# Kernel tuning notes

Hardware: AMD Instinct MI355X
Metric: run time of the kernel (lower is better)

Reference implementation:

```python
import jax, jax.numpy as jnp
import numpy as np

B, T = 64, 16384          # batch, frame_length
M, K = 8, 3               # memory_length, degree


def setup_inputs() -> dict:
    key = jax.random.key(0)
    k1, k2 = jax.random.split(key)
    x = jax.random.normal(k1, (B, T, 2), dtype=jnp.float32)
    h_0 = jnp.zeros((1,), dtype=jnp.float32)  # unused by the module, kept for signature fidelity
    Weight = jax.random.normal(k2, (M, 1 + K * M), dtype=jnp.float32) * 0.1
    return {"x": x, "h_0": h_0, "Weight": Weight}


def _gmp_forward(x, Weight):
    Bm, Tn, _ = x.shape
    Mm, Wd = Weight.shape
    Kk = (Wd - 1) // Mm
    cdt = jnp.complex64
    xc = jax.lax.complex(x[..., 0], x[..., 1])               # (B, T) complex
    zp = jnp.zeros((Bm, Mm - 1), dtype=cdt)
    xp = jnp.concatenate([zp, xc], axis=1)                   # (B, T+M-1): x padded by M-1 zeros
    # original code pads AGAIN before abs -> amp has a 2*(M-1)-zero prefix
    ap = jnp.abs(jnp.concatenate([zp, xp], axis=1))          # (B, T+2M-2) real
    # amp^(d+1) for d = 0..K-1  -> (B, K, T+2M-2)
    powers = ap[:, None, :] ** jnp.arange(1, Kk + 1, dtype=ap.dtype)[None, :, None]
    # sliding windows of xp: WX[b, j, i] = xp[b, j+i], i = 0..M-1  -> (B, T, M)
    WX = jnp.stack([xp[:, i:i + Tn] for i in range(Mm)], axis=-1)
    # Weight[:, 0] multiplies the raw window; Weight[:, 1:] reshaped to [tap i, lag m, degree d]
    W3 = Weight[:, 1:].reshape(Mm, Mm, Kk)
    out = jnp.einsum('i,bji->bj', Weight[:, 0].astype(cdt), WX)
    for m in range(Mm):  # structural loop over memory lags (M is small & fixed)
        # PWm[b, d, j, i] = amp_pad[b, j+m+i]^(d+1)  -> (B, K, T, M)
        PWm = jnp.stack([powers[:, :, m + i:m + i + Tn] for i in range(Mm)], axis=-1)
        out = out + jnp.einsum('bji,bdji,id->bj', WX, PWm.astype(cdt), W3[:, m, :].astype(cdt))
    return jnp.stack([jnp.real(out), jnp.imag(out)], axis=-1)  # (B, T, 2)


def reference(x, h_0, Weight):
    return _gmp_forward(x, Weight)
```

## Files before the change

kernel.cpp:

```cpp
#include <hip/hip_runtime.h>


#define B_SZ 64
#define T_SZ 16384
#define M_SZ 8
#define K_SZ 3
#define CHUNK 256
#define HALO 14
#define WIN (CHUNK + HALO)

__global__ __launch_bounds__(256) void gmp_kernel(const float* __restrict__ x,
                                                  const float* __restrict__ W,
                                                  float* __restrict__ out) {
    __shared__ float xre[WIN], xim[WIN], a1[WIN], a2[WIN], a3[WIN];
    const int tid   = threadIdx.x;
    const int chunk = blockIdx.x & 63;
    const int b     = blockIdx.x >> 6;
    const int j0    = chunk * CHUNK;

    for (int q = tid; q < WIN; q += 256) {
        const int g = j0 - HALO + q;
        float re = 0.f, im = 0.f;
        if (g >= 0) {
            const float2 v = ((const float2*)x)[(size_t)b * T_SZ + g];
            re = v.x; im = v.y;
        }
        const float s2 = fmaf(re, re, im * im);
        const float s1 = sqrtf(s2);
        xre[q] = re; xim[q] = im;
        a1[q] = s1; a2[q] = s2; a3[q] = s2 * s1;
    }
    __syncthreads();

    float accr = 0.f, acci = 0.f;
#pragma unroll
    for (int i = 0; i < M_SZ; ++i) {
        float c = W[i * 25];
#pragma unroll
        for (int m = 0; m < M_SZ; ++m) {
            const int q = tid + i + m;
            const int wb = i * 25 + 1 + m * 3;
            c = fmaf(W[wb + 0], a1[q], c);
            c = fmaf(W[wb + 1], a2[q], c);
            c = fmaf(W[wb + 2], a3[q], c);
        }
        const int qx = tid + i + 7;
        accr = fmaf(xre[qx], c, accr);
        acci = fmaf(xim[qx], c, acci);
    }

    const int j = j0 + tid;
    ((float2*)out)[(size_t)b * T_SZ + j] = make_float2(accr, acci);
}

extern "C" void kernel_launch(void* const* d_in, const int* in_sizes, int n_in,
                              void* d_out, int out_size, void* d_ws, size_t ws_size,
                              hipStream_t stream) {
    const float* x = (const float*)d_in[0];
    const float* W = (const float*)d_in[2];
    float* out = (float*)d_out;
    const int grid = B_SZ * (T_SZ / CHUNK);
    gmp_kernel<<<dim3(grid), dim3(256), 0, stream>>>(x, W, out);
}
```

Baseline: 70.51 us.

## Compute two outputs per thread with register-cached windows and Horner powers

```diff
diff --git a/kernel.cpp b/kernel.cpp
--- a/kernel.cpp
+++ b/kernel.cpp
@@ -3,54 +3,59 @@
 
 #define B_SZ 64
 #define T_SZ 16384
-#define M_SZ 8
-#define K_SZ 3
-#define CHUNK 256
+#define CHUNK 512
 #define HALO 14
 #define WIN (CHUNK + HALO)
 
 __global__ __launch_bounds__(256) void gmp_kernel(const float* __restrict__ x,
                                                   const float* __restrict__ W,
                                                   float* __restrict__ out) {
-    __shared__ float xre[WIN], xim[WIN], a1[WIN], a2[WIN], a3[WIN];
+    __shared__ float2 xs[WIN];
+    __shared__ float  as[WIN];
     const int tid   = threadIdx.x;
-    const int chunk = blockIdx.x & 63;
-    const int b     = blockIdx.x >> 6;
+    const int chunk = blockIdx.x & 31;
+    const int b     = blockIdx.x >> 5;
     const int j0    = chunk * CHUNK;
 
     for (int q = tid; q < WIN; q += 256) {
         const int g = j0 - HALO + q;
-        float re = 0.f, im = 0.f;
-        if (g >= 0) {
-            const float2 v = ((const float2*)x)[(size_t)b * T_SZ + g];
-            re = v.x; im = v.y;
-        }
-        const float s2 = fmaf(re, re, im * im);
-        const float s1 = sqrtf(s2);
-        xre[q] = re; xim[q] = im;
-        a1[q] = s1; a2[q] = s2; a3[q] = s2 * s1;
+        float2 v = make_float2(0.f, 0.f);
+        if (g >= 0) v = ((const float2*)x)[(size_t)b * T_SZ + g];
+        xs[q] = v;
+        as[q] = sqrtf(fmaf(v.x, v.x, v.y * v.y));
     }
     __syncthreads();
 
-    float accr = 0.f, acci = 0.f;
+    float av[16];
 #pragma unroll
-    for (int i = 0; i < M_SZ; ++i) {
-        float c = W[i * 25];
+    for (int k = 0; k < 16; ++k) av[k] = as[2 * tid + k];
+    float2 xv[9];
 #pragma unroll
-        for (int m = 0; m < M_SZ; ++m) {
-            const int q = tid + i + m;
-            const int wb = i * 25 + 1 + m * 3;
-            c = fmaf(W[wb + 0], a1[q], c);
-            c = fmaf(W[wb + 1], a2[q], c);
-            c = fmaf(W[wb + 2], a3[q], c);
+    for (int k = 0; k < 9; ++k) xv[k] = xs[2 * tid + 7 + k];
+
+    float ar0 = 0.f, ai0 = 0.f, ar1 = 0.f, ai1 = 0.f;
+#pragma unroll
+    for (int i = 0; i < 8; ++i) {
+        float c0 = W[i * 25];
+        float c1 = c0;
+#pragma unroll
+        for (int m = 0; m < 8; ++m) {
+            const float w1 = W[i * 25 + 1 + m * 3];
+            const float w2 = W[i * 25 + 2 + m * 3];
+            const float w3 = W[i * 25 + 3 + m * 3];
+            const float a0 = av[i + m];
+            const float a1 = av[i + m + 1];
+            float h0 = fmaf(a0, w3, w2);  h0 = fmaf(a0, h0, w1);  c0 = fmaf(a0, h0, c0);
+            float h1 = fmaf(a1, w3, w2);  h1 = fmaf(a1, h1, w1);  c1 = fmaf(a1, h1, c1);
         }
-        const int qx = tid + i + 7;
-        accr = fmaf(xre[qx], c, accr);
-        acci = fmaf(xim[qx], c, acci);
+        ar0 = fmaf(xv[i].x,     c0, ar0);
+        ai0 = fmaf(xv[i].y,     c0, ai0);
+        ar1 = fmaf(xv[i + 1].x, c1, ar1);
+        ai1 = fmaf(xv[i + 1].y, c1, ai1);
     }
 
-    const int j = j0 + tid;
-    ((float2*)out)[(size_t)b * T_SZ + j] = make_float2(accr, acci);
+    float4 o; o.x = ar0; o.y = ai0; o.z = ar1; o.w = ai1;
+    ((float4*)out)[((size_t)b * T_SZ + j0) / 2 + tid] = o;
 }
 
 extern "C" void kernel_launch(void* const* d_in, const int* in_sizes, int n_in,
```

Measured after the change: 68.08 us. 1.04x faster.
